# Kernel optimization log

Measured on AMD Instinct MI355X. Metric: run time of the kernel, lower is better.

Reference implementation:

```python
import jax, jax.numpy as jnp
import numpy as np

B, N, D = 4, 4096, 256


def setup_inputs() -> dict:
    key = jax.random.key(0)
    k1, k2 = jax.random.split(key)
    val = jax.random.normal(k1, (B, N, D), dtype=jnp.float32)
    state = jax.random.normal(k2, (B, N), dtype=jnp.float32)
    return {"val": val, "state": state}


def reference(val, state):
    # pairwise_fn: scaled dot-product -> scores [B, N, N]
    scale = val.shape[-1] ** -0.5
    scores = jnp.einsum("bid,bjd->bij", val, val) * scale
    # edge_compress_fn = softsign (non-softmax compression)
    edges = scores / (1.0 + jnp.abs(scores))
    # state_weight_edges=False, val/state projections are Identity
    delta_state = jnp.einsum("bij,bj->bi", edges, state)   # [B, N]
    delta_val = jnp.einsum("bij,bjd->bid", edges, val)      # [B, N, D]
    return (delta_state, delta_val)
```

## Files before the change

kernel.cpp:

```cpp
#include <hip/hip_runtime.h>


#define B_  4
#define N_  4096
#define D_  256

typedef __attribute__((ext_vector_type(8))) short short8;
typedef __attribute__((ext_vector_type(4))) float floatx4;

__device__ __forceinline__ unsigned short f2bf(float f) {
    unsigned int u = __float_as_uint(f);
    u += 0x7fff + ((u >> 16) & 1);
    return (unsigned short)(u >> 16);
}

__device__ __forceinline__ void gl_lds16(const void* g, void* l) {
    __builtin_amdgcn_global_load_lds(
        (const __attribute__((address_space(1))) unsigned int*)g,
        (__attribute__((address_space(3))) unsigned int*)l, 16, 0, 0);
}
__device__ __forceinline__ void gl_lds4(const void* g, void* l) {
    __builtin_amdgcn_global_load_lds(
        (const __attribute__((address_space(1))) unsigned int*)g,
        (__attribute__((address_space(3))) unsigned int*)l, 4, 0, 0);
}

__global__ __launch_bounds__(256)
void prepass_kernel(const float* __restrict__ val,
                    unsigned short* __restrict__ Vb,
                    unsigned short* __restrict__ VT) {
    __shared__ unsigned short tile[64][68];
    const int t   = threadIdx.x;
    const int blk = blockIdx.x;
    const int b   = blk >> 8;
    const int it  = (blk >> 2) & 63;
    const int dt  = blk & 3;
    const int i0  = it * 64, d0 = dt * 64;
    const float*    vb  = val + (size_t)b * N_ * D_;
    unsigned short* Vbb = Vb  + (size_t)b * N_ * D_;
    unsigned short* VTb = VT  + (size_t)b * D_ * N_;

    #pragma unroll
    for (int q = 0; q < 4; ++q) {
        int idx = t + 256 * q;
        int row = idx >> 4;
        int c4  = idx & 15;
        float4 v = *(const float4*)(vb + (size_t)(i0 + row) * D_ + d0 + c4 * 4);
        ushort4 h;
        h.x = f2bf(v.x); h.y = f2bf(v.y); h.z = f2bf(v.z); h.w = f2bf(v.w);
        *(ushort4*)(Vbb + (size_t)(i0 + row) * D_ + d0 + c4 * 4) = h;
        *(ushort4*)&tile[row][c4 * 4] = h;
    }
    __syncthreads();
    #pragma unroll
    for (int q = 0; q < 4; ++q) {
        int dr = (t >> 4) + q * 16;
        int i4 = t & 15;
        ushort4 h;
        h.x = tile[i4 * 4 + 0][dr];
        h.y = tile[i4 * 4 + 1][dr];
        h.z = tile[i4 * 4 + 2][dr];
        h.w = tile[i4 * 4 + 3][dr];
        *(ushort4*)(VTb + (size_t)(d0 + dr) * N_ + i0 + i4 * 4) = h;
    }
}

__global__ __launch_bounds__(512, 1)
void prop_main(const float* __restrict__ state,
               const unsigned short* __restrict__ Vb,
               const unsigned short* __restrict__ VT,
               float* __restrict__ dvp,
               float* __restrict__ dsp_o)
{
    __shared__ __attribute__((aligned(16))) unsigned char smem[136448];

    const int t    = threadIdx.x;
    const int g    = t >> 8;
    const int w    = t >> 6;
    const int w4   = w & 3;
    const int lane = t & 63;
    const int quad = lane >> 4;
    const int l16  = lane & 15;

    const int x   = blockIdx.x;
    const int b   = x >> 6;
    const int it  = (x >> 1) & 31;
    const int jh  = x & 1;
    const int it0 = it * 128;
    const int jbase = jh * 2048;
    const int niter = 32;

    unsigned short* vjL  = (unsigned short*)(smem + 65536);
    float*          stjL = (float*)(smem + 135168);
    float*          dsredg = (float*)(smem + 135424 + g * 512);

    const unsigned short* Vbb = Vb + (size_t)b * N_ * D_;
    const unsigned short* VTb = VT + (size_t)b * D_ * N_;
    const float*          stb = state + (size_t)b * N_;

    const int hi  = lane >> 5;
    const int p32 = lane & 31;
    const int dr8 = lane >> 3;
    const int p8  = lane & 7;

    int vgoff[4];
    int tgoff[4];
    #pragma unroll
    for (int n = 0; n < 4; ++n) {
        int r  = 2 * (w * 4 + n) + hi;
        vgoff[n] = r * 256 + (p32 ^ (r & 7)) * 8;
        int d  = 8 * (w * 4 + n) + dr8;
        tgoff[n] = d * 4096 + (p8 ^ dr8) * 8;
    }

    const int r0 = (w4 >> 1) * 32;
    const int c0 = (w4 & 1) * 32;
    const int pA = l16 & 7;

    short8 A0[8], A1[8];
    {
        const unsigned short* ar0 = Vbb + (size_t)(it0 + g * 64 + r0 + l16) * 256 + quad * 8;
        const unsigned short* ar1 = ar0 + 16 * 256;
        #pragma unroll
        for (int ks = 0; ks < 8; ++ks) {
            A0[ks] = *(const short8*)(ar0 + ks * 32);
            A1[ks] = *(const short8*)(ar1 + ks * 32);
        }
    }

    #pragma unroll
    for (int n = 0; n < 4; ++n)
        gl_lds16(VTb + (size_t)jbase + tgoff[n], smem + (w * 4 + n) * 1024);
    #pragma unroll
    for (int n = 0; n < 4; ++n)
        gl_lds16(Vbb + (size_t)jbase * 256 + vgoff[n],
                 smem + 65536 + (w * 4 + n) * 1024);
    if (w == 0) gl_lds4(stb + jbase + lane, stjL);

    floatx4 dv[4][4];
    #pragma unroll
    for (int a = 0; a < 4; ++a)
        #pragma unroll
        for (int c = 0; c < 4; ++c)
            dv[a][c] = (floatx4){0.f, 0.f, 0.f, 0.f};
    float dsp[2] = {0.f, 0.f};

    for (int k = 0; k < niter; ++k) {
        const int buf = k & 1;
        unsigned short* Eshg = (unsigned short*)(smem + 98304 + g * 18432 + buf * 9216);
        unsigned short* vjtg = (unsigned short*)(smem + buf * 32768);

        __syncthreads();

        if (k + 1 < niter) {
            const size_t j0n = jbase + (size_t)(k + 1) * 64;
            #pragma unroll
            for (int n = 0; n < 4; ++n)
                gl_lds16(VTb + j0n + tgoff[n],
                         smem + (buf ^ 1) * 32768 + (w * 4 + n) * 1024);
        }

        floatx4 sa[2][2];
        #pragma unroll
        for (int a = 0; a < 2; ++a)
            #pragma unroll
            for (int c = 0; c < 2; ++c)
                sa[a][c] = (floatx4){0.f, 0.f, 0.f, 0.f};

        #pragma unroll
        for (int ks = 0; ks < 8; ++ks) {
            const int p = ((ks * 4 + quad) ^ pA) * 8;
            short8 aj0 = *(const short8*)&vjL[(c0 + l16) * 256 + p];
            short8 aj1 = *(const short8*)&vjL[(c0 + 16 + l16) * 256 + p];
            sa[0][0] = __builtin_amdgcn_mfma_f32_16x16x32_bf16(aj0, A0[ks], sa[0][0], 0, 0, 0);
            sa[0][1] = __builtin_amdgcn_mfma_f32_16x16x32_bf16(aj0, A1[ks], sa[0][1], 0, 0, 0);
            sa[1][0] = __builtin_amdgcn_mfma_f32_16x16x32_bf16(aj1, A0[ks], sa[1][0], 0, 0, 0);
            sa[1][1] = __builtin_amdgcn_mfma_f32_16x16x32_bf16(aj1, A1[ks], sa[1][1], 0, 0, 0);
        }

        float4 stq[2];
        stq[0] = *(const float4*)&stjL[c0 + quad * 4];
        stq[1] = *(const float4*)&stjL[c0 + 16 + quad * 4];
        #pragma unroll
        for (int ja = 0; ja < 2; ++ja) {
            #pragma unroll
            for (int ic = 0; ic < 2; ++ic) {
                float e0 = sa[ja][ic][0] * __builtin_amdgcn_rcpf(16.0f + fabsf(sa[ja][ic][0]));
                float e1 = sa[ja][ic][1] * __builtin_amdgcn_rcpf(16.0f + fabsf(sa[ja][ic][1]));
                float e2 = sa[ja][ic][2] * __builtin_amdgcn_rcpf(16.0f + fabsf(sa[ja][ic][2]));
                float e3 = sa[ja][ic][3] * __builtin_amdgcn_rcpf(16.0f + fabsf(sa[ja][ic][3]));
                dsp[ic] += e0 * stq[ja].x + e1 * stq[ja].y + e2 * stq[ja].z + e3 * stq[ja].w;
                uint2 pk;
                pk.x = (unsigned int)f2bf(e0) | ((unsigned int)f2bf(e1) << 16);
                pk.y = (unsigned int)f2bf(e2) | ((unsigned int)f2bf(e3) << 16);
                *(uint2*)&Eshg[(r0 + ic * 16 + l16) * 72 + c0 + ja * 16 + quad * 4] = pk;
            }
        }
        __syncthreads();

        if (k + 1 < niter) {
            const size_t j0n = jbase + (size_t)(k + 1) * 64;
            #pragma unroll
            for (int n = 0; n < 4; ++n)
                gl_lds16(Vbb + j0n * 256 + vgoff[n],
                         smem + 65536 + (w * 4 + n) * 1024);
            if (w == 0) gl_lds4(stb + j0n + lane, stjL);
        }

        #pragma unroll
        for (int ks = 0; ks < 2; ++ks) {
            short8 af[4], bfr[4];
            #pragma unroll
            for (int a2 = 0; a2 < 4; ++a2)
                af[a2] = *(const short8*)&Eshg[(a2 * 16 + l16) * 72 + ks * 32 + quad * 8];
            #pragma unroll
            for (int c2 = 0; c2 < 4; ++c2) {
                const int d = w4 * 64 + c2 * 16 + l16;
                const int p = ((ks * 4 + quad) ^ pA) * 8;
                bfr[c2] = *(const short8*)&vjtg[d * 64 + p];
            }
            #pragma unroll
            for (int a2 = 0; a2 < 4; ++a2)
                #pragma unroll
                for (int c2 = 0; c2 < 4; ++c2)
                    dv[a2][c2] = __builtin_amdgcn_mfma_f32_16x16x32_bf16(af[a2], bfr[c2], dv[a2][c2], 0, 0, 0);
        }
    }

    float* dvo = dvp + (size_t)jh * B_ * N_ * D_ + (size_t)b * N_ * D_
                     + (size_t)(it0 + g * 64) * D_;
    #pragma unroll
    for (int a2 = 0; a2 < 4; ++a2)
        #pragma unroll
        for (int c2 = 0; c2 < 4; ++c2)
            #pragma unroll
            for (int r = 0; r < 4; ++r) {
                const int il = a2 * 16 + quad * 4 + r;
                const int d  = w4 * 64 + c2 * 16 + l16;
                dvo[(size_t)il * D_ + d] = dv[a2][c2][r];
            }

    #pragma unroll
    for (int ic = 0; ic < 2; ++ic) {
        float v = dsp[ic];
        v += __shfl_xor(v, 16);
        v += __shfl_xor(v, 32);
        dsp[ic] = v;
    }
    if (quad == 0) {
        #pragma unroll
        for (int ic = 0; ic < 2; ++ic)
            dsredg[(w4 & 1) * 64 + r0 + ic * 16 + l16] = dsp[ic];
    }
    __syncthreads();
    if (t < 128) {
        const int gg = t >> 6;
        const int i  = t & 63;
        const float* dsr = (const float*)(smem + 135424 + gg * 512);
        dsp_o[(size_t)jh * B_ * N_ + (size_t)b * N_ + it0 + gg * 64 + i]
            = dsr[i] + dsr[64 + i];
    }
}

__global__ __launch_bounds__(256)
void combine_kernel(const float4* __restrict__ dv0, const float4* __restrict__ dv1,
                    const float*  __restrict__ ds0, const float*  __restrict__ ds1,
                    float* __restrict__ out) {
    const int NDV4 = B_ * N_ * D_ / 4;
    const int NDS  = B_ * N_;
    int x = blockIdx.x * 256 + threadIdx.x;
    if (x < NDV4) {
        float4 a = dv0[x], c = dv1[x];
        float4 r;
        r.x = a.x + c.x; r.y = a.y + c.y; r.z = a.z + c.z; r.w = a.w + c.w;
        ((float4*)(out + NDS))[x] = r;
    } else {
        int y = (x - NDV4) * 4;
        if (y < NDS) {
            float4 a = *(const float4*)(ds0 + y);
            float4 c = *(const float4*)(ds1 + y);
            float4 r;
            r.x = a.x + c.x; r.y = a.y + c.y; r.z = a.z + c.z; r.w = a.w + c.w;
            *(float4*)(out + y) = r;
        }
    }
}

__global__ __launch_bounds__(256, 1)
void prop_kernel_fb(const float* __restrict__ val,
                    const float* __restrict__ state,
                    float* __restrict__ out) {
    __shared__ __attribute__((aligned(16))) unsigned short vi[64][264];
    __shared__ __attribute__((aligned(16))) unsigned short vj[64][264];
    __shared__ __attribute__((aligned(16))) unsigned short vjt[2048][8];
    __shared__ __attribute__((aligned(16))) unsigned short Esh[64][72];
    __shared__ float stj[64];
    __shared__ float dsred[2][64];

    const int t    = threadIdx.x;
    const int w    = t >> 6;
    const int lane = t & 63;
    const int quad = lane >> 4;
    const int l16  = lane & 15;
    const int b   = blockIdx.x >> 6;
    const int it0 = (blockIdx.x & 63) << 6;
    const float* valb = val   + (size_t)b * N_ * D_;
    const float* stb  = state + (size_t)b * N_;

    #pragma unroll
    for (int n = 0; n < 16; ++n) {
        int idx = t + 256 * n;
        int row = idx >> 6;
        int c4  = idx & 63;
        float4 v = *(const float4*)(valb + (size_t)(it0 + row) * D_ + c4 * 4);
        ushort4 h;
        h.x = f2bf(v.x); h.y = f2bf(v.y); h.z = f2bf(v.z); h.w = f2bf(v.w);
        *(ushort4*)&vi[row][c4 * 4] = h;
    }

    const int r0 = (w >> 1) * 32;
    const int c0 = (w & 1) * 32;
    floatx4 dv[4][4];
    #pragma unroll
    for (int a = 0; a < 4; ++a)
        #pragma unroll
        for (int c = 0; c < 4; ++c)
            dv[a][c] = (floatx4){0.f, 0.f, 0.f, 0.f};
    float dsp[8];
    #pragma unroll
    for (int k = 0; k < 8; ++k) dsp[k] = 0.f;

    for (int jt = 0; jt < 64; ++jt) {
        const int j0 = jt * 64;
        #pragma unroll
        for (int n = 0; n < 16; ++n) {
            int idx = t + 256 * n;
            int row = idx >> 6;
            int c4  = idx & 63;
            float4 v = *(const float4*)(valb + (size_t)(j0 + row) * D_ + c4 * 4);
            ushort4 h;
            h.x = f2bf(v.x); h.y = f2bf(v.y); h.z = f2bf(v.z); h.w = f2bf(v.w);
            *(ushort4*)&vj[row][c4 * 4] = h;
        }
        if (t < 64) stj[t] = stb[j0 + t];
        __syncthreads();

        #pragma unroll
        for (int n = 0; n < 8; ++n) {
            const int d  = t;
            const int jb = n;
            short8 pk;
            #pragma unroll
            for (int jj = 0; jj < 8; ++jj) pk[jj] = (short)vj[jb * 8 + jj][d];
            *(short8*)&vjt[d * 8 + (jb ^ (d & 7))][0] = pk;
        }

        floatx4 sa[2][2];
        #pragma unroll
        for (int a = 0; a < 2; ++a)
            #pragma unroll
            for (int c = 0; c < 2; ++c)
                sa[a][c] = (floatx4){0.f, 0.f, 0.f, 0.f};
        #pragma unroll
        for (int ks = 0; ks < 8; ++ks) {
            const int d0 = ks * 32 + quad * 8;
            short8 a0 = *(const short8*)&vi[r0 + l16][d0];
            short8 a1 = *(const short8*)&vi[r0 + 16 + l16][d0];
            short8 b0 = *(const short8*)&vj[c0 + l16][d0];
            short8 b1 = *(const short8*)&vj[c0 + 16 + l16][d0];
            sa[0][0] = __builtin_amdgcn_mfma_f32_16x16x32_bf16(a0, b0, sa[0][0], 0, 0, 0);
            sa[0][1] = __builtin_amdgcn_mfma_f32_16x16x32_bf16(a0, b1, sa[0][1], 0, 0, 0);
            sa[1][0] = __builtin_amdgcn_mfma_f32_16x16x32_bf16(a1, b0, sa[1][0], 0, 0, 0);
            sa[1][1] = __builtin_amdgcn_mfma_f32_16x16x32_bf16(a1, b1, sa[1][1], 0, 0, 0);
        }

        float stc0 = stj[c0 + l16];
        float stc1 = stj[c0 + 16 + l16];
        #pragma unroll
        for (int a = 0; a < 2; ++a) {
            #pragma unroll
            for (int r = 0; r < 4; ++r) {
                const int il = r0 + a * 16 + quad * 4 + r;
                float s0 = sa[a][0][r] * 0.0625f;
                float s1 = sa[a][1][r] * 0.0625f;
                float e0 = s0 / (1.0f + fabsf(s0));
                float e1 = s1 / (1.0f + fabsf(s1));
                dsp[a * 4 + r] += e0 * stc0 + e1 * stc1;
                Esh[il][c0 + l16]      = f2bf(e0);
                Esh[il][c0 + 16 + l16] = f2bf(e1);
            }
        }
        __syncthreads();

        #pragma unroll
        for (int ks = 0; ks < 2; ++ks) {
            short8 af[4], bfr[4];
            #pragma unroll
            for (int a2 = 0; a2 < 4; ++a2)
                af[a2] = *(const short8*)&Esh[a2 * 16 + l16][ks * 32 + quad * 8];
            #pragma unroll
            for (int c2 = 0; c2 < 4; ++c2) {
                const int d  = w * 64 + c2 * 16 + l16;
                const int jb = ks * 4 + quad;
                bfr[c2] = *(const short8*)&vjt[d * 8 + (jb ^ (d & 7))][0];
            }
            #pragma unroll
            for (int a2 = 0; a2 < 4; ++a2)
                #pragma unroll
                for (int c2 = 0; c2 < 4; ++c2)
                    dv[a2][c2] = __builtin_amdgcn_mfma_f32_16x16x32_bf16(af[a2], bfr[c2], dv[a2][c2], 0, 0, 0);
        }
    }

    float* dvo = out + (size_t)B_ * N_ + (size_t)b * N_ * D_;
    #pragma unroll
    for (int a2 = 0; a2 < 4; ++a2)
        #pragma unroll
        for (int c2 = 0; c2 < 4; ++c2)
            #pragma unroll
            for (int r = 0; r < 4; ++r) {
                const int i = it0 + a2 * 16 + quad * 4 + r;
                const int d = w * 64 + c2 * 16 + l16;
                dvo[(size_t)i * D_ + d] = dv[a2][c2][r];
            }

    #pragma unroll
    for (int k = 0; k < 8; ++k) {
        float v = dsp[k];
        v += __shfl_xor(v, 1);
        v += __shfl_xor(v, 2);
        v += __shfl_xor(v, 4);
        v += __shfl_xor(v, 8);
        dsp[k] = v;
    }
    if (l16 == 0) {
        #pragma unroll
        for (int a = 0; a < 2; ++a)
            #pragma unroll
            for (int r = 0; r < 4; ++r) {
                const int row = (w >> 1) * 32 + a * 16 + quad * 4 + r;
                dsred[w & 1][row] = dsp[a * 4 + r];
            }
    }
    __syncthreads();
    if (t < 64) out[(size_t)b * N_ + it0 + t] = dsred[0][t] + dsred[1][t];
}

extern "C" void kernel_launch(void* const* d_in, const int* in_sizes, int n_in,
                              void* d_out, int out_size, void* d_ws, size_t ws_size,
                              hipStream_t stream) {
    const float* val   = (const float*)d_in[0];
    const float* state = (const float*)d_in[1];
    float* out = (float*)d_out;

    const size_t nE         = (size_t)B_ * N_ * D_;
    const size_t need_base  = 2 * nE * sizeof(unsigned short);
    const size_t need_split = need_base + 2 * nE * sizeof(float)
                            + 2 * (size_t)B_ * N_ * sizeof(float);

    if (ws_size >= need_split) {
        unsigned short* Vb = (unsigned short*)d_ws;
        unsigned short* VT = Vb + nE;
        float* dvp = (float*)(VT + nE);
        float* dsp = dvp + 2 * nE;
        prepass_kernel<<<dim3(1024), dim3(256), 0, stream>>>(val, Vb, VT);
        prop_main<<<dim3(256), dim3(512), 0, stream>>>(state, Vb, VT, dvp, dsp);
        const int NDV4 = B_ * N_ * D_ / 4;
        const int NDS4 = B_ * N_ / 4;
        combine_kernel<<<dim3((NDV4 + NDS4) / 256), dim3(256), 0, stream>>>(
            (const float4*)dvp, (const float4*)(dvp + nE),
            dsp, dsp + (size_t)B_ * N_, out);
    } else {
        prop_kernel_fb<<<dim3(256), dim3(256), 0, stream>>>(val, state, out);
    }
}
```

Measured before the change: 151.5 us.

## Load transposed V fragments directly to registers and double-buffer V rows in LDS

The transposed V operand for the second GEMM is now loaded from global memory straight into registers (double-buffered across iterations) instead of being staged through LDS. The freed LDS space is used to double-buffer the V row tiles and state, so their prefetch can be issued before the first barrier rather than after the second. This removes LDS traffic and shrinks shared memory use, but it adds 32 registers per lane and relies on register prefetch latency being hidden by one iteration of compute.

Result: slower. 299.9 us (+97.9%).

```diff
diff --git a/kernel.cpp b/kernel.cpp
--- a/kernel.cpp
+++ b/kernel.cpp
@@ -72,7 +72,7 @@
                float* __restrict__ dvp,
                float* __restrict__ dsp_o)
 {
-    __shared__ __attribute__((aligned(16))) unsigned char smem[136448];
+    __shared__ __attribute__((aligned(16))) unsigned char smem[103936];
 
     const int t    = threadIdx.x;
     const int g    = t >> 8;
@@ -90,27 +90,18 @@
     const int jbase = jh * 2048;
     const int niter = 32;
 
-    unsigned short* vjL  = (unsigned short*)(smem + 65536);
-    float*          stjL = (float*)(smem + 135168);
-    float*          dsredg = (float*)(smem + 135424 + g * 512);
-
     const unsigned short* Vbb = Vb + (size_t)b * N_ * D_;
     const unsigned short* VTb = VT + (size_t)b * D_ * N_;
     const float*          stb = state + (size_t)b * N_;
 
     const int hi  = lane >> 5;
     const int p32 = lane & 31;
-    const int dr8 = lane >> 3;
-    const int p8  = lane & 7;
 
     int vgoff[4];
-    int tgoff[4];
     #pragma unroll
     for (int n = 0; n < 4; ++n) {
         int r  = 2 * (w * 4 + n) + hi;
         vgoff[n] = r * 256 + (p32 ^ (r & 7)) * 8;
-        int d  = 8 * (w * 4 + n) + dr8;
-        tgoff[n] = d * 4096 + (p8 ^ dr8) * 8;
     }
 
     const int r0 = (w4 >> 1) * 32;
@@ -128,14 +119,23 @@
         }
     }
 
+    const unsigned short* gB[4];
+    #pragma unroll
+    for (int c2 = 0; c2 < 4; ++c2)
+        gB[c2] = VTb + (size_t)(w4 * 64 + c2 * 16 + l16) * 4096
+                     + jbase + quad * 8;
+
     #pragma unroll
     for (int n = 0; n < 4; ++n)
-        gl_lds16(VTb + (size_t)jbase + tgoff[n], smem + (w * 4 + n) * 1024);
-    #pragma unroll
-    for (int n = 0; n < 4; ++n)
-        gl_lds16(Vbb + (size_t)jbase * 256 + vgoff[n],
-                 smem + 65536 + (w * 4 + n) * 1024);
-    if (w == 0) gl_lds4(stb + jbase + lane, stjL);
+        gl_lds16(Vbb + (size_t)jbase * 256 + vgoff[n], smem + (w * 4 + n) * 1024);
+    if (w == 0) gl_lds4(stb + jbase + lane, smem + 102400);
+
+    short8 Bf[2][8];
+    #pragma unroll
+    for (int ks = 0; ks < 2; ++ks)
+        #pragma unroll
+        for (int c2 = 0; c2 < 4; ++c2)
+            Bf[0][ks * 4 + c2] = *(const short8*)(gB[c2] + ks * 32);
 
     floatx4 dv[4][4];
     #pragma unroll
@@ -147,8 +147,9 @@
 
     for (int k = 0; k < niter; ++k) {
         const int buf = k & 1;
-        unsigned short* Eshg = (unsigned short*)(smem + 98304 + g * 18432 + buf * 9216);
-        unsigned short* vjtg = (unsigned short*)(smem + buf * 32768);
+        unsigned short* Eshg = (unsigned short*)(smem + 65536 + g * 18432 + buf * 9216);
+        const unsigned short* vjL = (const unsigned short*)(smem + buf * 32768);
+        const float* stjL = (const float*)(smem + 102400 + buf * 256);
 
         __syncthreads();
 
@@ -156,8 +157,16 @@
             const size_t j0n = jbase + (size_t)(k + 1) * 64;
             #pragma unroll
             for (int n = 0; n < 4; ++n)
-                gl_lds16(VTb + j0n + tgoff[n],
+                gl_lds16(Vbb + j0n * 256 + vgoff[n],
                          smem + (buf ^ 1) * 32768 + (w * 4 + n) * 1024);
+            if (w == 0) gl_lds4(stb + j0n + lane, smem + 102400 + (buf ^ 1) * 256);
+            const int joff = (k + 1) * 64;
+            #pragma unroll
+            for (int ks = 0; ks < 2; ++ks)
+                #pragma unroll
+                for (int c2 = 0; c2 < 4; ++c2)
+                    Bf[buf ^ 1][ks * 4 + c2] =
+                        *(const short8*)(gB[c2] + joff + ks * 32);
         }
 
         floatx4 sa[2][2];
@@ -198,32 +207,18 @@
         }
         __syncthreads();
 
-        if (k + 1 < niter) {
-            const size_t j0n = jbase + (size_t)(k + 1) * 64;
-            #pragma unroll
-            for (int n = 0; n < 4; ++n)
-                gl_lds16(Vbb + j0n * 256 + vgoff[n],
-                         smem + 65536 + (w * 4 + n) * 1024);
-            if (w == 0) gl_lds4(stb + j0n + lane, stjL);
-        }
-
         #pragma unroll
         for (int ks = 0; ks < 2; ++ks) {
-            short8 af[4], bfr[4];
+            short8 af[4];
             #pragma unroll
             for (int a2 = 0; a2 < 4; ++a2)
                 af[a2] = *(const short8*)&Eshg[(a2 * 16 + l16) * 72 + ks * 32 + quad * 8];
-            #pragma unroll
-            for (int c2 = 0; c2 < 4; ++c2) {
-                const int d = w4 * 64 + c2 * 16 + l16;
-                const int p = ((ks * 4 + quad) ^ pA) * 8;
-                bfr[c2] = *(const short8*)&vjtg[d * 64 + p];
-            }
             #pragma unroll
             for (int a2 = 0; a2 < 4; ++a2)
                 #pragma unroll
                 for (int c2 = 0; c2 < 4; ++c2)
-                    dv[a2][c2] = __builtin_amdgcn_mfma_f32_16x16x32_bf16(af[a2], bfr[c2], dv[a2][c2], 0, 0, 0);
+                    dv[a2][c2] = __builtin_amdgcn_mfma_f32_16x16x32_bf16(
+                        af[a2], Bf[buf][ks * 4 + c2], dv[a2][c2], 0, 0, 0);
         }
     }
 
@@ -247,6 +242,7 @@
         v += __shfl_xor(v, 32);
         dsp[ic] = v;
     }
+    float* dsredg = (float*)(smem + 102912 + g * 512);
     if (quad == 0) {
         #pragma unroll
         for (int ic = 0; ic < 2; ++ic)
@@ -256,7 +252,7 @@
     if (t < 128) {
         const int gg = t >> 6;
         const int i  = t & 63;
-        const float* dsr = (const float*)(smem + 135424 + gg * 512);
+        const float* dsr = (const float*)(smem + 102912 + gg * 512);
         dsp_o[(size_t)jh * B_ * N_ + (size_t)b * N_ + it0 + gg * 64 + i]
             = dsr[i] + dsr[64 + i];
     }
```
